# Optimization experiments

Measured on AMD Instinct MI355X. Metric: run time of the kernel, lower is better.

Reference implementation:

```python
import jax, jax.numpy as jnp
import numpy as np

K = 64                      # sort-pool k
B_GRAPHS, N_PER = 256, 512  # graphs, nodes per graph
DIM_F, E_PER = 128, 8192    # node feature dim, edges per graph
EMB = 32


def setup_inputs() -> dict:
    key = jax.random.key(0)
    ks = jax.random.split(key, 12)
    N = B_GRAPHS * N_PER
    off = (jnp.arange(B_GRAPHS) * N_PER)[:, None]
    x = jax.random.normal(ks[0], (N, DIM_F), jnp.float32)
    edge_src = (jax.random.randint(ks[1], (B_GRAPHS, E_PER), 0, N_PER) + off).reshape(-1)
    edge_dst = (jax.random.randint(ks[2], (B_GRAPHS, E_PER), 0, N_PER) + off).reshape(-1)

    def lin(k, o, i):
        return (jax.random.normal(k, (o, i), jnp.float32) / np.float32(np.sqrt(i)))

    return {
        "x": x,
        "W0": lin(ks[3], EMB, DIM_F), "b0": jnp.zeros((EMB,), jnp.float32),
        "W1": lin(ks[4], EMB, EMB),   "b1": jnp.zeros((EMB,), jnp.float32),
        "W2": lin(ks[5], EMB, EMB),   "b2": jnp.zeros((EMB,), jnp.float32),
        "W3": lin(ks[6], 1, EMB),     "b3": jnp.zeros((1,), jnp.float32),
        "conv1_w": jax.random.normal(ks[7], (16, 1, 97), jnp.float32) / np.float32(np.sqrt(97.0)),
        "conv1_b": jnp.zeros((16,), jnp.float32),
        "conv2_w": jax.random.normal(ks[8], (32, 16, 5), jnp.float32) / np.float32(np.sqrt(80.0)),
        "conv2_b": jnp.zeros((32,), jnp.float32),
        "d1_w": lin(ks[9], 128, 896),  "d1_b": jnp.zeros((128,), jnp.float32),
        "d2_w": lin(ks[10], 10, 128),  "d2_b": jnp.zeros((10,), jnp.float32),
        "edge_src": edge_src, "edge_dst": edge_dst,
        "num_graphs": B_GRAPHS,
    }


def _dgcnn_conv(h_in, W, b, src, dst):
    # h = lin(x); message = (1/deg_src)[dst] * h[src]; scatter-add at dst
    N = h_in.shape[0]
    h = h_in @ W.T + b
    deg = jax.ops.segment_sum(jnp.ones_like(src, dtype=h.dtype), src, num_segments=N)
    norm = 1.0 / deg                       # self-loops guarantee deg >= 1
    msg = h[src] * norm[dst][:, None]      # [E+N, C]
    return jax.ops.segment_sum(msg, dst, num_segments=N)


def _forward(x, W0, b0, W1, b1, W2, b2, W3, b3,
             conv1_w, conv1_b, conv2_w, conv2_b,
             d1_w, d1_b, d2_w, d2_b, src, dst, num_graphs):
    N = x.shape[0]
    self_idx = jnp.arange(N)
    src = jnp.concatenate([src, self_idx])   # add_self_loops
    dst = jnp.concatenate([dst, self_idx])
    hs = []
    h = x
    for (W, b) in ((W0, b0), (W1, b1), (W2, b2), (W3, b3)):
        h = jnp.tanh(_dgcnn_conv(h, W, b, src, dst))
        hs.append(h)
    feat = jnp.concatenate(hs, axis=1)       # [N, 97]
    D = feat.shape[1]
    B = num_graphs
    n = N // B
    g = feat.reshape(B, n, D)
    # global_sort_pool: sort nodes per graph by last channel, descending, take top-k
    order = jnp.argsort(-g[:, :, -1], axis=1)[:, :K]
    topk = jnp.take_along_axis(g, order[:, :, None], axis=1)   # [B, K, D]
    # Conv1d(1,16,kernel=D,stride=D) over [B,1,K*D] == per-node linear on D
    c1 = jax.nn.relu(jnp.einsum('bkd,od->bok', topk, conv1_w[:, 0, :])
                     + conv1_b[None, :, None])                  # [B,16,K]
    p = c1.reshape(B, 16, K // 2, 2).max(axis=-1)               # MaxPool1d(2,2)
    c2 = jax.lax.conv_general_dilated(p, conv2_w, (1,), 'VALID',
                                      dimension_numbers=('NCH', 'OIH', 'NCH'))
    c2 = jax.nn.relu(c2 + conv2_b[None, :, None])               # [B,32,28]
    flat = c2.reshape(B, -1)                                    # [B,896]
    hid = jax.nn.relu(flat @ d1_w.T + d1_b)                     # dropout = identity (eval)
    return hid @ d2_w.T + d2_b                                  # [B,10]


def reference(x, W0, b0, W1, b1, W2, b2, W3, b3,
              conv1_w, conv1_b, conv2_w, conv2_b,
              d1_w, d1_b, d2_w, d2_b, edge_src, edge_dst, num_graphs):
    return _forward(x, W0, b0, W1, b1, W2, b2, W3, b3,
                    conv1_w, conv1_b, conv2_w, conv2_b,
                    d1_w, d1_b, d2_w, d2_b, edge_src, edge_dst, num_graphs)
```

## Files before the change

### kernel.cpp

```cpp
#include <hip/hip_runtime.h>

#define NG   256
#define NP   512
#define EPG  8192
#define FDIM 128
#define STB  36

#define OFF_STAGE 0
#define OFF_BUFB  65536
#define OFF_CSR   139264
#define OFF_OFFS  155648
#define OFF_WT    156680
#define OFF_CUR   156712
#define OFF_DCNT  158760
#define OFF_NRM   160808
#define SMEM_SZ   162856

#define OFF_KEY  OFF_CSR
#define OFF_IDX  (OFF_CSR + 2048)
#define OFF_L3   OFF_CUR
#define FO_FEAT 0
#define FO_C1   6208
#define FO_P    7232
#define FO_C2   7744
#define FO_HID  8640

__global__ __launch_bounds__(1024, 4) void dgcnn_fused(
    const float* __restrict__ x,
    const float* __restrict__ W0, const float* __restrict__ b0,
    const float* __restrict__ W1, const float* __restrict__ b1,
    const float* __restrict__ W2, const float* __restrict__ b2,
    const float* __restrict__ W3, const float* __restrict__ b3,
    const float* __restrict__ c1w, const float* __restrict__ c1b,
    const float* __restrict__ c2w, const float* __restrict__ c2b,
    const float* __restrict__ d1w, const float* __restrict__ d1b,
    const float* __restrict__ d2w, const float* __restrict__ d2b,
    const int* __restrict__ esrc, const int* __restrict__ edst,
    float* __restrict__ hs1, float* __restrict__ hs2,
    float* __restrict__ out)
{
  extern __shared__ char smem[];
  float*          stageF = (float*)(smem + OFF_STAGE);
  float*          bufB  = (float*)(smem + OFF_BUFB);
  unsigned short* csr   = (unsigned short*)(smem + OFF_CSR);
  unsigned short* offs  = (unsigned short*)(smem + OFF_OFFS);
  unsigned int*   wt    = (unsigned int*)(smem + OFF_WT);
  unsigned int*   cur   = (unsigned int*)(smem + OFF_CUR);
  unsigned int*   dcnt  = (unsigned int*)(smem + OFF_DCNT);
  float*          nrm   = (float*)(smem + OFF_NRM);
  float*          lin3S = (float*)(smem + OFF_L3);
  float*          keyA  = (float*)(smem + OFF_KEY);
  unsigned int*   idxA  = (unsigned int*)(smem + OFF_IDX);

  const int g    = blockIdx.x;
  const int tid  = threadIdx.x;
  const int lane = tid & 63;
  const int wv   = __builtin_amdgcn_readfirstlane(tid >> 6);
  const int half = __builtin_amdgcn_readfirstlane(tid >> 9);
  const int v    = tid & 511;
  const int nb   = g * NP;
  const size_t gb = (size_t)g * (NP * 32);

  const int ldRow0 = tid >> 3;
  const int ldGrp  = tid & 7;
  const int ldSwz  = (ldGrp ^ (ldRow0 & 7)) * 16;
  const float* xp0 = x + (size_t)nb * FDIM + ldGrp * 4 + (size_t)(ldRow0      ) * FDIM;
  const float* xp1 = x + (size_t)nb * FDIM + ldGrp * 4 + (size_t)(ldRow0 + 128) * FDIM;
  const float* xp2 = x + (size_t)nb * FDIM + ldGrp * 4 + (size_t)(ldRow0 + 256) * FDIM;
  const float* xp3 = x + (size_t)nb * FDIM + ldGrp * 4 + (size_t)(ldRow0 + 384) * FDIM;
  char* sp0 = smem + OFF_STAGE + (ldRow0      ) * 128 + ldSwz;
  char* sp1 = smem + OFF_STAGE + (ldRow0 + 128) * 128 + ldSwz;
  char* sp2 = smem + OFF_STAGE + (ldRow0 + 256) * 128 + ldSwz;
  char* sp3 = smem + OFF_STAGE + (ldRow0 + 384) * 128 + ldSwz;
#define LOADC(kc, r0, r1, r2, r3)                         \
  { r0 = *(const float4*)(xp0 + (kc) * 32);               \
    r1 = *(const float4*)(xp1 + (kc) * 32);               \
    r2 = *(const float4*)(xp2 + (kc) * 32);               \
    r3 = *(const float4*)(xp3 + (kc) * 32); }
#define STOREC(r0, r1, r2, r3)                            \
  { *(float4*)sp0 = r0; *(float4*)sp1 = r1;               \
    *(float4*)sp2 = r2; *(float4*)sp3 = r3; }

  float4 xA0, xA1, xA2, xA3, xB0, xB1, xB2, xB3;
  LOADC(0, xA0, xA1, xA2, xA3);

  if (tid < 512) { cur[tid] = 0u; dcnt[tid] = 0u; }
  __syncthreads();

  int es[8], ed[8];
  {
    const int eb = g * EPG;
    const int4* s4 = (const int4*)(esrc + eb);
    const int4* d4 = (const int4*)(edst + eb);
    const int4 sa = s4[tid], sb = s4[tid + 1024];
    const int4 da = d4[tid], db = d4[tid + 1024];
    es[0]=sa.x-nb; es[1]=sa.y-nb; es[2]=sa.z-nb; es[3]=sa.w-nb;
    es[4]=sb.x-nb; es[5]=sb.y-nb; es[6]=sb.z-nb; es[7]=sb.w-nb;
    ed[0]=da.x-nb; ed[1]=da.y-nb; ed[2]=da.z-nb; ed[3]=da.w-nb;
    ed[4]=db.x-nb; ed[5]=db.y-nb; ed[6]=db.z-nb; ed[7]=db.w-nb;
#pragma unroll
    for (int i = 0; i < 8; i++) {
      atomicAdd(&dcnt[es[i]], 1u);
      atomicAdd(&dcnt[ed[i]], 65536u);
    }
  }
  __syncthreads();

  unsigned c_scan = 0;
  if (tid < 512) {
    const unsigned cw = dcnt[tid];
    nrm[tid] = 1.0f / (float)((cw & 0xFFFFu) + 1u);
    c_scan = cw >> 16;
    for (int d = 1; d < 64; d <<= 1) {
      const unsigned t = __shfl_up(c_scan, (unsigned)d, 64);
      if (lane >= d) c_scan += t;
    }
    if (lane == 63) wt[wv] = c_scan;
  }
  __syncthreads();
  if (tid < 512) {
    unsigned base = 0;
    for (int w = 0; w < wv; w++) base += wt[w];
    offs[tid + 1] = (unsigned short)(base + c_scan);
    if (tid == 0) offs[0] = 0;
  }
  __syncthreads();

#pragma unroll
  for (int i = 0; i < 8; i++) {
    const unsigned pos = (unsigned)offs[ed[i]] + atomicAdd(&cur[ed[i]], 1u);
    csr[pos] = (unsigned short)es[i];
  }

  float acc0[16];
#pragma unroll
  for (int c = 0; c < 16; c++) acc0[c] = b0[half * 16 + c];
  const char* rowp = smem + OFF_STAGE + v * 128;
  const int vswz = v & 7;
  auto compute_chunk = [&](int kc) {
#pragma unroll
    for (int jg = 0; jg < 8; jg++) {
      const float4 t = *(const float4*)(rowp + ((jg ^ vswz) * 16));
#pragma unroll
      for (int c = 0; c < 16; c++) {
        const float* wr = W0 + (size_t)(half * 16 + c) * FDIM + kc * 32 + jg * 4;
        acc0[c] = fmaf(t.x, wr[0], acc0[c]);
        acc0[c] = fmaf(t.y, wr[1], acc0[c]);
        acc0[c] = fmaf(t.z, wr[2], acc0[c]);
        acc0[c] = fmaf(t.w, wr[3], acc0[c]);
      }
    }
  };
  STOREC(xA0, xA1, xA2, xA3);
  LOADC(1, xB0, xB1, xB2, xB3);
  __syncthreads();
  compute_chunk(0);
  __syncthreads();
  STOREC(xB0, xB1, xB2, xB3);
  LOADC(2, xA0, xA1, xA2, xA3);
  __syncthreads();
  compute_chunk(1);
  __syncthreads();
  STOREC(xA0, xA1, xA2, xA3);
  LOADC(3, xB0, xB1, xB2, xB3);
  __syncthreads();
  compute_chunk(2);
  __syncthreads();
  STOREC(xB0, xB1, xB2, xB3);
  __syncthreads();
  compute_chunk(3);
  {
    float4* br = (float4*)(bufB + v * STB + half * 16);
#pragma unroll
    for (int j = 0; j < 4; j++)
      br[j] = make_float4(acc0[j*4+0], acc0[j*4+1], acc0[j*4+2], acc0[j*4+3]);
  }
  __syncthreads();

  float h[16];
  auto do_agg = [&]() {
    float4 A0, A1, A2, A3;
    const float4* sr = (const float4*)(bufB + v * STB + half * 16);
    A0 = sr[0]; A1 = sr[1]; A2 = sr[2]; A3 = sr[3];
    const int e0 = offs[v], e1 = offs[v + 1];
    int e = e0;
    for (; e + 1 < e1; e += 2) {
      const int s0 = csr[e], s1 = csr[e + 1];
      const float4* rb0 = (const float4*)(bufB + s0 * STB + half * 16);
      const float4* rb1 = (const float4*)(bufB + s1 * STB + half * 16);
      const float4 p0 = rb0[0], p1 = rb0[1], p2 = rb0[2], p3 = rb0[3];
      const float4 q0 = rb1[0], q1 = rb1[1], q2 = rb1[2], q3 = rb1[3];
      A0.x += p0.x + q0.x; A0.y += p0.y + q0.y; A0.z += p0.z + q0.z; A0.w += p0.w + q0.w;
      A1.x += p1.x + q1.x; A1.y += p1.y + q1.y; A1.z += p1.z + q1.z; A1.w += p1.w + q1.w;
      A2.x += p2.x + q2.x; A2.y += p2.y + q2.y; A2.z += p2.z + q2.z; A2.w += p2.w + q2.w;
      A3.x += p3.x + q3.x; A3.y += p3.y + q3.y; A3.z += p3.z + q3.z; A3.w += p3.w + q3.w;
    }
    if (e < e1) {
      const int s = csr[e];
      const float4* rb = (const float4*)(bufB + s * STB + half * 16);
      const float4 r0 = rb[0], r1 = rb[1], r2 = rb[2], r3 = rb[3];
      A0.x += r0.x; A0.y += r0.y; A0.z += r0.z; A0.w += r0.w;
      A1.x += r1.x; A1.y += r1.y; A1.z += r1.z; A1.w += r1.w;
      A2.x += r2.x; A2.y += r2.y; A2.z += r2.z; A2.w += r2.w;
      A3.x += r3.x; A3.y += r3.y; A3.z += r3.z; A3.w += r3.w;
    }
    const float nv = nrm[v];
    h[0]=tanhf(A0.x*nv); h[1]=tanhf(A0.y*nv); h[2]=tanhf(A0.z*nv); h[3]=tanhf(A0.w*nv);
    h[4]=tanhf(A1.x*nv); h[5]=tanhf(A1.y*nv); h[6]=tanhf(A1.z*nv); h[7]=tanhf(A1.w*nv);
    h[8]=tanhf(A2.x*nv); h[9]=tanhf(A2.y*nv); h[10]=tanhf(A2.z*nv); h[11]=tanhf(A2.w*nv);
    h[12]=tanhf(A3.x*nv); h[13]=tanhf(A3.y*nv); h[14]=tanhf(A3.z*nv); h[15]=tanhf(A3.w*nv);
  };

  auto put_h = [&]() {
    float4* br = (float4*)(bufB + v * STB + half * 16);
#pragma unroll
    for (int j = 0; j < 4; j++)
      br[j] = make_float4(h[j*4+0], h[j*4+1], h[j*4+2], h[j*4+3]);
  };

  auto spill = [&](float* dst) {
#pragma unroll
    for (int c = 0; c < 16; c++)
      dst[gb + (size_t)(half * 16 + c) * 512 + v] = h[c];
  };

  auto do_lin = [&](const float* __restrict__ W, const float* __restrict__ b) {
    float hf[32];
    const float4* rr = (const float4*)(bufB + v * STB);
#pragma unroll
    for (int j = 0; j < 8; j++) {
      const float4 t = rr[j];
      hf[j*4+0]=t.x; hf[j*4+1]=t.y; hf[j*4+2]=t.z; hf[j*4+3]=t.w;
    }
    __syncthreads();
    float acc[16];
#pragma unroll
    for (int c = 0; c < 16; c++) {
      const int C = half * 16 + c;
      const float* wr = W + C * 32;
      float a = b[C];
#pragma unroll
      for (int j = 0; j < 32; j++) a = fmaf(hf[j], wr[j], a);
      acc[c] = a;
    }
    float4* br = (float4*)(bufB + v * STB + half * 16);
#pragma unroll
    for (int j = 0; j < 4; j++)
      br[j] = make_float4(acc[j*4+0], acc[j*4+1], acc[j*4+2], acc[j*4+3]);
    __syncthreads();
  };

  do_agg();
  __syncthreads();
  put_h(); spill(hs1);
  __syncthreads();
  do_lin(W1, b1);
  do_agg();
  __syncthreads();
  put_h(); spill(hs2);
  __syncthreads();
  do_lin(W2, b2);
  do_agg();
  __syncthreads();
  put_h();
  __syncthreads();

  if (tid < 512) {
    const float4* rr = (const float4*)(bufB + tid * STB);
    double a = (double)b3[0];
#pragma unroll
    for (int j = 0; j < 8; j++) {
      const float4 t = rr[j];
      a = fma((double)t.x, (double)W3[j*4+0], a);
      a = fma((double)t.y, (double)W3[j*4+1], a);
      a = fma((double)t.z, (double)W3[j*4+2], a);
      a = fma((double)t.w, (double)W3[j*4+3], a);
    }
    lin3S[tid] = (float)a;
  }
  __syncthreads();
  float h4 = 0.f;
  if (tid < 512) {
    double a = (double)lin3S[tid];
    const int e0 = offs[tid], e1 = offs[tid + 1];
    for (int e = e0; e < e1; e++) a += (double)lin3S[csr[e]];
    a *= (double)nrm[tid];
    h4 = tanhf((float)a);
  }
  __syncthreads();

  if (tid < 512) {
    float    sk = h4;
    unsigned si = (unsigned)tid;
#pragma unroll
    for (int kk = 2; kk <= 64; kk <<= 1) {
#pragma unroll
      for (int j = kk >> 1; j > 0; j >>= 1) {
        const float    pk = __shfl_xor(sk, j, 64);
        const unsigned pi = __shfl_xor(si, j, 64);
        const bool amFirst = (sk > pk) || (sk == pk && si < pi);
        const bool lower   = (lane & j) == 0;
        const bool dir     = (tid & kk) == 0;
        const bool keepMine = (lower == dir) ? amFirst : !amFirst;
        if (!keepMine) { sk = pk; si = pi; }
      }
    }
    keyA[tid] = sk;
    idxA[tid] = si;
  }
  for (int k = 128; k <= NP; k <<= 1) {
    for (int j = k >> 1; j > 0; j >>= 1) {
      __syncthreads();
      if (tid < 512) {
        const int i = tid;
        const int l = i ^ j;
        if (l > i) {
          const float    ki = keyA[i], kl = keyA[l];
          const unsigned ii = idxA[i], il = idxA[l];
          const bool iBeforeL = (ki > kl) || (ki == kl && ii < il);
          const bool doSwap = ((i & k) == 0) ? (!iBeforeL) : iBeforeL;
          if (doSwap) {
            keyA[i] = kl; keyA[l] = ki;
            idxA[i] = il; idxA[l] = ii;
          }
        }
      }
    }
  }
  __syncthreads();

  {
    float* featS = stageF + FO_FEAT;
    const int k = tid >> 4, t = tid & 15;
    const int node = (int)idxA[k];
#pragma unroll
    for (int m = 0; m < 7; m++) {
      const int d = t + 16 * m;
      float val;
      if (d < 32)       val = hs1[gb + (size_t)d * 512 + node];
      else if (d < 64)  val = hs2[gb + (size_t)(d - 32) * 512 + node];
      else if (d < 96)  val = bufB[node * STB + (d - 64)];
      else              val = keyA[k];
      if (d < 97) featS[d * 64 + k] = val;
    }
  }
  __syncthreads();

  {
    const float* featS = stageF + FO_FEAT;
    float* c1s = stageF + FO_C1;
    const int ch = wv;
    float a = c1b[ch];
    const float* wr = c1w + ch * 97;
    for (int d = 0; d < 97; d++)
      a = fmaf(featS[d * 64 + lane], wr[d], a);
    c1s[ch * 64 + lane] = fmaxf(a, 0.f);
  }
  __syncthreads();

  if (tid < 512) {
    const float* c1s = stageF + FO_C1;
    float* ps  = stageF + FO_P;
    const int o = tid >> 5, jj = tid & 31;
    ps[o * 32 + jj] = fmaxf(c1s[o * 64 + 2 * jj], c1s[o * 64 + 2 * jj + 1]);
  }
  __syncthreads();

  {
    const float* ps  = stageF + FO_P;
    float* c2s = stageF + FO_C2;
    const int o = wv;
    if (lane < 28) {
      float a0 = 0.f, a1 = 0.f;
      for (int i = 0; i < 16; i++) {
#pragma unroll
        for (int r = 0; r < 5; r++) {
          const float pv = ps[i * 32 + lane + r];
          a0 = fmaf(pv, c2w[((o     ) * 16 + i) * 5 + r], a0);
          a1 = fmaf(pv, c2w[((o + 16) * 16 + i) * 5 + r], a1);
        }
      }
      c2s[(o     ) * 28 + lane] = fmaxf(a0 + c2b[o     ], 0.f);
      c2s[(o + 16) * 28 + lane] = fmaxf(a1 + c2b[o + 16], 0.f);
    }
  }
  __syncthreads();

  {
    const float* c2s  = stageF + FO_C2;
    float* hids = stageF + FO_HID;
    float fl[14];
#pragma unroll
    for (int j = 0; j < 14; j++) fl[j] = c2s[lane + j * 64];
    for (int hh = 0; hh < 8; hh++) {
      const int hI = wv * 8 + hh;
      const float* wr = d1w + (size_t)hI * 896;
      float a = 0.f;
#pragma unroll
      for (int j = 0; j < 14; j++) a = fmaf(fl[j], wr[lane + j * 64], a);
#pragma unroll
      for (int m = 32; m > 0; m >>= 1) a += __shfl_xor(a, m, 64);
      if (lane == 0) hids[hI] = fmaxf(a + d1b[hI], 0.f);
    }
  }
  __syncthreads();

  if (tid < 10) {
    const float* hids = stageF + FO_HID;
    const float* wr = d2w + tid * 128;
    float a = d2b[tid];
#pragma unroll 8
    for (int hh = 0; hh < 128; hh++) a = fmaf(hids[hh], wr[hh], a);
    out[g * 10 + tid] = a;
  }
}

extern "C" void kernel_launch(void* const* d_in, const int* in_sizes, int n_in,
                              void* d_out, int out_size, void* d_ws, size_t ws_size,
                              hipStream_t stream) {
  const float* x   = (const float*)d_in[0];
  const float* W0  = (const float*)d_in[1];
  const float* b0  = (const float*)d_in[2];
  const float* W1  = (const float*)d_in[3];
  const float* b1  = (const float*)d_in[4];
  const float* W2  = (const float*)d_in[5];
  const float* b2  = (const float*)d_in[6];
  const float* W3  = (const float*)d_in[7];
  const float* b3  = (const float*)d_in[8];
  const float* c1w = (const float*)d_in[9];
  const float* c1b = (const float*)d_in[10];
  const float* c2w = (const float*)d_in[11];
  const float* c2b = (const float*)d_in[12];
  const float* d1w = (const float*)d_in[13];
  const float* d1b = (const float*)d_in[14];
  const float* d2w = (const float*)d_in[15];
  const float* d2b = (const float*)d_in[16];
  const int* esrc  = (const int*)d_in[17];
  const int* edst  = (const int*)d_in[18];

  float* hs1 = (float*)d_ws;
  float* hs2 = hs1 + (size_t)NG * NP * 32;
  float* outp = (float*)d_out;

  hipFuncSetAttribute(reinterpret_cast<const void*>(dgcnn_fused),
                      hipFuncAttributeMaxDynamicSharedMemorySize, SMEM_SZ);
  dgcnn_fused<<<NG, 1024, SMEM_SZ, stream>>>(x, W0, b0, W1, b1, W2, b2, W3, b3,
                                             c1w, c1b, c2w, c2b, d1w, d1b, d2w, d2b,
                                             esrc, edst, hs1, hs2, outp);
}
```

Baseline: 288.9 us.

## Double-buffer layer features, cut barriers, replace block-wide bitonic sort with top-64 wave merges

Aggregated features now go to a separate padded buffer (bufA, stride 33), so the linear layer reads its own half from registers and only the other half from shared memory, which removes several __syncthreads per layer. The block-wide bitonic stages over all 512 nodes (many barriers) are replaced by per-wave sorts of 64 plus three rounds of top-64 bitonic merges between waves, since only the top K=64 nodes are needed. The cursor array is folded into dcnt to save shared memory. The cost is a more complex layout and the risk of ordering or tie-breaking differences in the merge.

```diff
diff --git a/kernel.cpp b/kernel.cpp
--- a/kernel.cpp
+++ b/kernel.cpp
@@ -4,21 +4,22 @@
 #define NP   512
 #define EPG  8192
 #define FDIM 128
+#define STA  33
 #define STB  36
 
-#define OFF_STAGE 0
-#define OFF_BUFB  65536
-#define OFF_CSR   139264
-#define OFF_OFFS  155648
-#define OFF_WT    156680
-#define OFF_CUR   156712
+#define OFF_BUFA  0
+#define OFF_BUFB  67584
+#define OFF_CSR   141312
+#define OFF_OFFS  157696
+#define OFF_WT    158728
 #define OFF_DCNT  158760
 #define OFF_NRM   160808
 #define SMEM_SZ   162856
 
-#define OFF_KEY  OFF_CSR
-#define OFF_IDX  (OFF_CSR + 2048)
-#define OFF_L3   OFF_CUR
+#define OFF_KEYA OFF_CSR
+#define OFF_IDXA (OFF_CSR + 2048)
+#define OFF_KEYB (OFF_CSR + 4096)
+#define OFF_IDXB (OFF_CSR + 6144)
 #define FO_FEAT 0
 #define FO_C1   6208
 #define FO_P    7232
@@ -40,17 +41,19 @@
     float* __restrict__ out)
 {
   extern __shared__ char smem[];
-  float*          stageF = (float*)(smem + OFF_STAGE);
+  float*          stageF = (float*)(smem + OFF_BUFA);
+  float*          bufA  = (float*)(smem + OFF_BUFA);
   float*          bufB  = (float*)(smem + OFF_BUFB);
   unsigned short* csr   = (unsigned short*)(smem + OFF_CSR);
   unsigned short* offs  = (unsigned short*)(smem + OFF_OFFS);
   unsigned int*   wt    = (unsigned int*)(smem + OFF_WT);
-  unsigned int*   cur   = (unsigned int*)(smem + OFF_CUR);
   unsigned int*   dcnt  = (unsigned int*)(smem + OFF_DCNT);
   float*          nrm   = (float*)(smem + OFF_NRM);
-  float*          lin3S = (float*)(smem + OFF_L3);
-  float*          keyA  = (float*)(smem + OFF_KEY);
-  unsigned int*   idxA  = (unsigned int*)(smem + OFF_IDX);
+  float*          lin3S = (float*)(smem + OFF_DCNT);
+  float*          keyA  = (float*)(smem + OFF_KEYA);
+  unsigned int*   idxA  = (unsigned int*)(smem + OFF_IDXA);
+  float*          keyB  = (float*)(smem + OFF_KEYB);
+  unsigned int*   idxB  = (unsigned int*)(smem + OFF_IDXB);
 
   const int g    = blockIdx.x;
   const int tid  = threadIdx.x;
@@ -68,10 +71,10 @@
   const float* xp1 = x + (size_t)nb * FDIM + ldGrp * 4 + (size_t)(ldRow0 + 128) * FDIM;
   const float* xp2 = x + (size_t)nb * FDIM + ldGrp * 4 + (size_t)(ldRow0 + 256) * FDIM;
   const float* xp3 = x + (size_t)nb * FDIM + ldGrp * 4 + (size_t)(ldRow0 + 384) * FDIM;
-  char* sp0 = smem + OFF_STAGE + (ldRow0      ) * 128 + ldSwz;
-  char* sp1 = smem + OFF_STAGE + (ldRow0 + 128) * 128 + ldSwz;
-  char* sp2 = smem + OFF_STAGE + (ldRow0 + 256) * 128 + ldSwz;
-  char* sp3 = smem + OFF_STAGE + (ldRow0 + 384) * 128 + ldSwz;
+  char* sp0 = smem + OFF_BUFA + (ldRow0      ) * 128 + ldSwz;
+  char* sp1 = smem + OFF_BUFA + (ldRow0 + 128) * 128 + ldSwz;
+  char* sp2 = smem + OFF_BUFA + (ldRow0 + 256) * 128 + ldSwz;
+  char* sp3 = smem + OFF_BUFA + (ldRow0 + 384) * 128 + ldSwz;
 #define LOADC(kc, r0, r1, r2, r3)                         \
   { r0 = *(const float4*)(xp0 + (kc) * 32);               \
     r1 = *(const float4*)(xp1 + (kc) * 32);               \
@@ -84,7 +87,7 @@
   float4 xA0, xA1, xA2, xA3, xB0, xB1, xB2, xB3;
   LOADC(0, xA0, xA1, xA2, xA3);
 
-  if (tid < 512) { cur[tid] = 0u; dcnt[tid] = 0u; }
+  if (tid < 512) dcnt[tid] = 0u;
   __syncthreads();
 
   int es[8], ed[8];
@@ -110,6 +113,7 @@
   if (tid < 512) {
     const unsigned cw = dcnt[tid];
     nrm[tid] = 1.0f / (float)((cw & 0xFFFFu) + 1u);
+    dcnt[tid] = 0u;
     c_scan = cw >> 16;
     for (int d = 1; d < 64; d <<= 1) {
       const unsigned t = __shfl_up(c_scan, (unsigned)d, 64);
@@ -128,14 +132,14 @@
 
 #pragma unroll
   for (int i = 0; i < 8; i++) {
-    const unsigned pos = (unsigned)offs[ed[i]] + atomicAdd(&cur[ed[i]], 1u);
+    const unsigned pos = (unsigned)offs[ed[i]] + atomicAdd(&dcnt[ed[i]], 1u);
     csr[pos] = (unsigned short)es[i];
   }
 
   float acc0[16];
 #pragma unroll
   for (int c = 0; c < 16; c++) acc0[c] = b0[half * 16 + c];
-  const char* rowp = smem + OFF_STAGE + v * 128;
+  const char* rowp = smem + OFF_BUFA + v * 128;
   const int vswz = v & 7;
   auto compute_chunk = [&](int kc) {
 #pragma unroll
@@ -211,11 +215,10 @@
     h[12]=tanhf(A3.x*nv); h[13]=tanhf(A3.y*nv); h[14]=tanhf(A3.z*nv); h[15]=tanhf(A3.w*nv);
   };
 
-  auto put_h = [&]() {
-    float4* br = (float4*)(bufB + v * STB + half * 16);
-#pragma unroll
-    for (int j = 0; j < 4; j++)
-      br[j] = make_float4(h[j*4+0], h[j*4+1], h[j*4+2], h[j*4+3]);
+  auto put_hA = [&]() {
+    float* aw = bufA + v * STA + half * 16;
+#pragma unroll
+    for (int j = 0; j < 16; j++) aw[j] = h[j];
   };
 
   auto spill = [&](float* dst) {
@@ -225,14 +228,10 @@
   };
 
   auto do_lin = [&](const float* __restrict__ W, const float* __restrict__ b) {
-    float hf[32];
-    const float4* rr = (const float4*)(bufB + v * STB);
-#pragma unroll
-    for (int j = 0; j < 8; j++) {
-      const float4 t = rr[j];
-      hf[j*4+0]=t.x; hf[j*4+1]=t.y; hf[j*4+2]=t.z; hf[j*4+3]=t.w;
-    }
-    __syncthreads();
+    float hf[16];
+    const float* ar = bufA + v * STA + (half ^ 1) * 16;
+#pragma unroll
+    for (int j = 0; j < 16; j++) hf[j] = ar[j];
     float acc[16];
 #pragma unroll
     for (int c = 0; c < 16; c++) {
@@ -240,42 +239,36 @@
       const float* wr = W + C * 32;
       float a = b[C];
 #pragma unroll
-      for (int j = 0; j < 32; j++) a = fmaf(hf[j], wr[j], a);
+      for (int j = 0; j < 16; j++) a = fmaf(h[j],  wr[half * 16 + j], a);
+#pragma unroll
+      for (int j = 0; j < 16; j++) a = fmaf(hf[j], wr[(half ^ 1) * 16 + j], a);
       acc[c] = a;
     }
     float4* br = (float4*)(bufB + v * STB + half * 16);
 #pragma unroll
     for (int j = 0; j < 4; j++)
       br[j] = make_float4(acc[j*4+0], acc[j*4+1], acc[j*4+2], acc[j*4+3]);
-    __syncthreads();
   };
 
   do_agg();
-  __syncthreads();
-  put_h(); spill(hs1);
+  put_hA(); spill(hs1);
   __syncthreads();
   do_lin(W1, b1);
+  __syncthreads();
   do_agg();
-  __syncthreads();
-  put_h(); spill(hs2);
+  put_hA(); spill(hs2);
   __syncthreads();
   do_lin(W2, b2);
+  __syncthreads();
   do_agg();
-  __syncthreads();
-  put_h();
-  __syncthreads();
-
-  if (tid < 512) {
-    const float4* rr = (const float4*)(bufB + tid * STB);
+  put_hA();
+  __syncthreads();
+
+  if (tid < 512) {
+    const float* ar = bufA + tid * STA;
     double a = (double)b3[0];
 #pragma unroll
-    for (int j = 0; j < 8; j++) {
-      const float4 t = rr[j];
-      a = fma((double)t.x, (double)W3[j*4+0], a);
-      a = fma((double)t.y, (double)W3[j*4+1], a);
-      a = fma((double)t.z, (double)W3[j*4+2], a);
-      a = fma((double)t.w, (double)W3[j*4+3], a);
-    }
+    for (int j = 0; j < 32; j++) a = fma((double)ar[j], (double)W3[j], a);
     lin3S[tid] = (float)a;
   }
   __syncthreads();
@@ -300,7 +293,7 @@
         const unsigned pi = __shfl_xor(si, j, 64);
         const bool amFirst = (sk > pk) || (sk == pk && si < pi);
         const bool lower   = (lane & j) == 0;
-        const bool dir     = (tid & kk) == 0;
+        const bool dir     = (lane & kk) == 0;
         const bool keepMine = (lower == dir) ? amFirst : !amFirst;
         if (!keepMine) { sk = pk; si = pi; }
       }
@@ -308,40 +301,55 @@
     keyA[tid] = sk;
     idxA[tid] = si;
   }
-  for (int k = 128; k <= NP; k <<= 1) {
-    for (int j = k >> 1; j > 0; j >>= 1) {
-      __syncthreads();
-      if (tid < 512) {
-        const int i = tid;
-        const int l = i ^ j;
-        if (l > i) {
-          const float    ki = keyA[i], kl = keyA[l];
-          const unsigned ii = idxA[i], il = idxA[l];
-          const bool iBeforeL = (ki > kl) || (ki == kl && ii < il);
-          const bool doSwap = ((i & k) == 0) ? (!iBeforeL) : iBeforeL;
-          if (doSwap) {
-            keyA[i] = kl; keyA[l] = ki;
-            idxA[i] = il; idxA[l] = ii;
-          }
-        }
-      }
-    }
-  }
+  __syncthreads();
+
+  auto merge_round = [&](const float* kin, const unsigned* iin,
+                         float* kout, unsigned* iout, int L, int R, int O) {
+    float    ak = kin[L * 64 + lane];
+    unsigned ai = iin[L * 64 + lane];
+    float    bk = kin[R * 64 + 63 - lane];
+    unsigned bi = iin[R * 64 + 63 - lane];
+    float mk; unsigned mi;
+    if ((ak > bk) || (ak == bk && ai < bi)) { mk = ak; mi = ai; }
+    else                                    { mk = bk; mi = bi; }
+#pragma unroll
+    for (int j = 32; j > 0; j >>= 1) {
+      const float    pk = __shfl_xor(mk, j, 64);
+      const unsigned pi = __shfl_xor(mi, j, 64);
+      const bool amF   = (mk > pk) || (mk == pk && mi < pi);
+      const bool lower = (lane & j) == 0;
+      if (lower != amF) { mk = pk; mi = pi; }
+    }
+    kout[O * 64 + lane] = mk;
+    iout[O * 64 + lane] = mi;
+  };
+  if (wv < 4) merge_round(keyA, idxA, keyB, idxB, 2 * wv, 2 * wv + 1, wv);
+  __syncthreads();
+  if (wv < 2) merge_round(keyB, idxB, keyA, idxA, 2 * wv, 2 * wv + 1, wv);
+  __syncthreads();
+  if (wv == 0) merge_round(keyA, idxA, keyB, idxB, 0, 1, 0);
   __syncthreads();
 
   {
     float* featS = stageF + FO_FEAT;
     const int k = tid >> 4, t = tid & 15;
-    const int node = (int)idxA[k];
+    const int node = (int)idxB[k];
+    float vals[7];
 #pragma unroll
     for (int m = 0; m < 7; m++) {
       const int d = t + 16 * m;
-      float val;
+      float val = 0.f;
       if (d < 32)       val = hs1[gb + (size_t)d * 512 + node];
       else if (d < 64)  val = hs2[gb + (size_t)(d - 32) * 512 + node];
-      else if (d < 96)  val = bufB[node * STB + (d - 64)];
-      else              val = keyA[k];
-      if (d < 97) featS[d * 64 + k] = val;
+      else if (d < 96)  val = bufA[node * STA + (d - 64)];
+      else              val = keyB[k];
+      vals[m] = val;
+    }
+    __syncthreads();
+#pragma unroll
+    for (int m = 0; m < 7; m++) {
+      const int d = t + 16 * m;
+      if (d < 97) featS[d * 64 + k] = vals[m];
     }
   }
   __syncthreads();
```

Result: no change. 287.0 us (-0.7%).
